# Performance work log

Measured on AMD Instinct MI355X. Metric: run time of the kernel, lower is better.

The kernel has to match this reference:

```python
import jax, jax.numpy as jnp
import numpy as np

B, T, D, H, K = 64, 2000, 512, 256, 5


def setup_inputs() -> dict:
    key = jax.random.key(0)
    ks = jax.random.split(key, 4)
    state = jax.random.normal(ks[0], (B, 1, D), dtype=jnp.float32)
    enc_z = jax.random.normal(ks[1], (B, T, D), dtype=jnp.float32)
    # small init scale keeps exp(param_net(state)) numerically tame
    W1 = jax.random.normal(ks[2], (D, H), dtype=jnp.float32) * 0.05
    b1 = jnp.zeros((H,), dtype=jnp.float32)
    W2 = jax.random.normal(ks[3], (H, 3 * K), dtype=jnp.float32) * 0.05
    b2 = jnp.zeros((3 * K,), dtype=jnp.float32)
    return {"state": state, "enc_z": enc_z, "W1": W1, "b1": b1, "W2": W2, "b2": b2}


def reference(state, enc_z, W1, b1, W2, b2):
    # param_net: Linear -> Tanh -> Linear, then exp (all params positive)
    h = jnp.tanh(state @ W1 + b1)                 # [B,1,H]
    params = jnp.exp(h @ W2 + b2)                 # [B,1,3K]
    means = params[..., 0::3]                     # [B,1,K]  (gather of indices 3i)
    scales = params[..., 1::3]                    # [B,1,K]  (indices 3i+1)
    w = params[..., 2::3]                         # [B,1,K]  (indices 3i+2)
    # NOTE: original applies softmax over dim=1 (the singleton dim) -> all ones.
    weights = jax.nn.softmax(w, axis=1)           # [B,1,K] == ones (faithful)
    t = enc_z.shape[1]
    j = jnp.arange(t, dtype=enc_z.dtype)[None, :, None]  # [1,T,1]
    cdf = lambda x: jax.nn.sigmoid((x - means) / scales)  # broadcasts -> [B,T,K]
    probs = weights * (cdf(j + 0.5) - cdf(j - 0.5))        # [B,T,K]
    align = jnp.sum(probs, axis=2)                          # [B,T]
    context = jnp.einsum('bt,btd->bd', align, enc_z)[:, None, :]  # [B,1,D]
    return context
```

## Files before the change

### kernel.cpp

```cpp
#include <hip/hip_runtime.h>
#include <math.h>

#define BB 64
#define TT 2000
#define DD 512
#define HH 256
#define KK 5
#define PP (3*KK)
#define D4 (DD/4)


__global__ __launch_bounds__(1024) void mlp_params_kernel(
    const float* __restrict__ state,
    const float* __restrict__ W1,
    const float* __restrict__ b1,
    const float* __restrict__ W2,
    const float* __restrict__ b2,
    float* __restrict__ ws_params)
{
    const int b     = blockIdx.x;
    const int tid   = threadIdx.x;
    const int q     = tid & 63;
    const int slice = tid >> 6;

    __shared__ float s_state[DD];
    __shared__ float s_part[16][HH];
    __shared__ float hs[HH];
    __shared__ float s_red[16][17];
    __shared__ float pr[PP];

    if (tid < DD) s_state[tid] = state[(size_t)b * DD + tid];
    __syncthreads();

    {
        const float4* w1v = (const float4*)W1;
        const int d0 = slice * 32;
        float4 acc = make_float4(0.f, 0.f, 0.f, 0.f);
        #pragma unroll 16
        for (int dd = 0; dd < 32; ++dd) {
            const int d    = d0 + dd;
            const float s  = s_state[d];
            const float4 w = w1v[(size_t)d * 64 + q];
            acc.x += s * w.x; acc.y += s * w.y;
            acc.z += s * w.z; acc.w += s * w.w;
        }
        s_part[slice][4*q+0] = acc.x;
        s_part[slice][4*q+1] = acc.y;
        s_part[slice][4*q+2] = acc.z;
        s_part[slice][4*q+3] = acc.w;
    }
    __syncthreads();

    if (tid < HH) {
        float a = b1[tid];
        #pragma unroll
        for (int s = 0; s < 16; ++s) a += s_part[s][tid];
        hs[tid] = tanhf(a);
    }
    __syncthreads();

    if (tid < 256) {
        const int p = tid >> 4;
        const int g = tid & 15;
        float a = 0.f;
        if (p < PP) {
            #pragma unroll
            for (int i = 0; i < 16; ++i)
                a += hs[g + 16*i] * W2[(size_t)(g + 16*i) * PP + p];
        }
        s_red[p][g] = a;
    }
    __syncthreads();
    if (tid < PP) {
        float a = b2[tid];
        #pragma unroll
        for (int g = 0; g < 16; ++g) a += s_red[tid][g];
        pr[tid] = expf(a);
    }
    __syncthreads();

    if (tid == 0) {
        float tc = 1.0f;
        #pragma unroll
        for (int k = 0; k < KK; ++k)
            tc = fmaxf(tc, pr[3*k] + 36.0f * pr[3*k+1] + 1.0f);
        ws_params[(size_t)b * 16 + 15] = tc;
    }
    if (tid < KK) {
        ws_params[(size_t)b * 16 + tid]     = pr[3*tid];
        ws_params[(size_t)b * 16 + 8 + tid] = 1.0f / pr[3*tid + 1];
    }
}

__global__ __launch_bounds__(512) void context_kernel(
    const float* __restrict__ enc_z,
    const float* __restrict__ ws_params,
    float* __restrict__ out)
{
    const int b   = blockIdx.x;
    const int tid = threadIdx.x;
    const int h   = tid >> 7;
    const int col = tid & 127;

    __shared__ float pr[16];
    __shared__ float al[TT];
    __shared__ float s_acc[4][DD];

    if (tid < 16) pr[tid] = ws_params[(size_t)b * 16 + tid];
    __syncthreads();

    const int Tact = min(TT, (int)ceilf(pr[15]));

    for (int t = tid; t < Tact; t += 512) {
        const float tf = (float)t;
        float a = 0.0f;
        #pragma unroll
        for (int k = 0; k < KK; ++k) {
            const float m  = pr[k];
            const float is = pr[8 + k];
            const float hi = (tf + 0.5f - m) * is;
            const float lo = (tf - 0.5f - m) * is;
            a += 1.0f / (1.0f + expf(-hi)) - 1.0f / (1.0f + expf(-lo));
        }
        al[t] = a;
    }
    __syncthreads();

    const float4* e4 = (const float4*)enc_z + (size_t)b * TT * D4 + col;
    float ax = 0.f, ay = 0.f, az = 0.f, aw = 0.f;
    #pragma unroll 4
    for (int t = h; t < Tact; t += 4) {
        const float a  = al[t];
        const float4 v = e4[(size_t)t * D4];
        ax += a * v.x; ay += a * v.y; az += a * v.z; aw += a * v.w;
    }
    s_acc[h][4*col+0] = ax;
    s_acc[h][4*col+1] = ay;
    s_acc[h][4*col+2] = az;
    s_acc[h][4*col+3] = aw;
    __syncthreads();

    if (tid < 128) {
        float4 r;
        r.x = s_acc[0][4*tid+0] + s_acc[1][4*tid+0] + s_acc[2][4*tid+0] + s_acc[3][4*tid+0];
        r.y = s_acc[0][4*tid+1] + s_acc[1][4*tid+1] + s_acc[2][4*tid+1] + s_acc[3][4*tid+1];
        r.z = s_acc[0][4*tid+2] + s_acc[1][4*tid+2] + s_acc[2][4*tid+2] + s_acc[3][4*tid+2];
        r.w = s_acc[0][4*tid+3] + s_acc[1][4*tid+3] + s_acc[2][4*tid+3] + s_acc[3][4*tid+3];
        ((float4*)out)[(size_t)b * D4 + tid] = r;
    }
}

extern "C" void kernel_launch(void* const* d_in, const int* in_sizes, int n_in,
                              void* d_out, int out_size, void* d_ws, size_t ws_size,
                              hipStream_t stream) {
    const float* state = (const float*)d_in[0];
    const float* enc_z = (const float*)d_in[1];
    const float* W1    = (const float*)d_in[2];
    const float* b1    = (const float*)d_in[3];
    const float* W2    = (const float*)d_in[4];
    const float* b2    = (const float*)d_in[5];
    float* out = (float*)d_out;

    float* ws_params = (float*)d_ws;

    mlp_params_kernel<<<BB, 1024, 0, stream>>>(state, W1, b1, W2, b2, ws_params);
    context_kernel<<<BB, 512, 0, stream>>>(enc_z, ws_params, out);
}
```

Baseline: 16.31 us.

## Split first MLP layer across blocks and fuse second layer into context kernel

The first linear layer now runs in a separate kernel launched with four blocks per batch row. Each block reduces one 128-wide slice of the input dimension and writes partial hidden sums to workspace. The tanh, the second layer, exp and the parameter extraction move into the start of the context kernel, so parameters no longer make a round trip through global memory. This spreads the W1 reads over more compute units and shortens the serial chain in the first kernel. In exchange, the context kernel repeats a small amount of MLP work per block.

Result: faster. 15.53 us (-4.8%).

```diff
diff --git a/kernel.cpp b/kernel.cpp
--- a/kernel.cpp
+++ b/kernel.cpp
@@ -8,54 +8,72 @@
 #define KK 5
 #define PP (3*KK)
 #define D4 (DD/4)
+#define NSL 4
 
 
-__global__ __launch_bounds__(1024) void mlp_params_kernel(
+__global__ __launch_bounds__(256) void h_partial_kernel(
     const float* __restrict__ state,
     const float* __restrict__ W1,
+    float* __restrict__ hpart)
+{
+    const int blk = blockIdx.x;
+    const int b   = blk >> 2;
+    const int s   = blk & 3;
+    const int tid = threadIdx.x;
+    const int q   = tid & 63;
+    const int r   = tid >> 6;
+
+    __shared__ float sst[128];
+    __shared__ float s_part[4][HH];
+
+    if (tid < 128) sst[tid] = state[(size_t)b * DD + s * 128 + tid];
+    __syncthreads();
+
+    const float4* w1v = (const float4*)W1;
+    float4 acc = make_float4(0.f, 0.f, 0.f, 0.f);
+    #pragma unroll 8
+    for (int it = 0; it < 32; ++it) {
+        const int dl = it * 4 + r;
+        const int d  = s * 128 + dl;
+        const float sv  = sst[dl];
+        const float4 w  = w1v[(size_t)d * 64 + q];
+        acc.x += sv * w.x; acc.y += sv * w.y;
+        acc.z += sv * w.z; acc.w += sv * w.w;
+    }
+    s_part[r][4*q+0] = acc.x;
+    s_part[r][4*q+1] = acc.y;
+    s_part[r][4*q+2] = acc.z;
+    s_part[r][4*q+3] = acc.w;
+    __syncthreads();
+
+    if (tid < HH)
+        hpart[((size_t)b * NSL + s) * HH + tid] =
+            s_part[0][tid] + s_part[1][tid] + s_part[2][tid] + s_part[3][tid];
+}
+
+__global__ __launch_bounds__(512) void context_kernel(
+    const float* __restrict__ enc_z,
+    const float* __restrict__ hpart,
     const float* __restrict__ b1,
     const float* __restrict__ W2,
     const float* __restrict__ b2,
-    float* __restrict__ ws_params)
+    float* __restrict__ out)
 {
-    const int b     = blockIdx.x;
-    const int tid   = threadIdx.x;
-    const int q     = tid & 63;
-    const int slice = tid >> 6;
+    const int b   = blockIdx.x;
+    const int tid = threadIdx.x;
+    const int h   = tid >> 7;
+    const int col = tid & 127;
 
-    __shared__ float s_state[DD];
-    __shared__ float s_part[16][HH];
     __shared__ float hs[HH];
     __shared__ float s_red[16][17];
     __shared__ float pr[PP];
-
-    if (tid < DD) s_state[tid] = state[(size_t)b * DD + tid];
-    __syncthreads();
-
-    {
-        const float4* w1v = (const float4*)W1;
-        const int d0 = slice * 32;
-        float4 acc = make_float4(0.f, 0.f, 0.f, 0.f);
-        #pragma unroll 16
-        for (int dd = 0; dd < 32; ++dd) {
-            const int d    = d0 + dd;
-            const float s  = s_state[d];
-            const float4 w = w1v[(size_t)d * 64 + q];
-            acc.x += s * w.x; acc.y += s * w.y;
-            acc.z += s * w.z; acc.w += s * w.w;
-        }
-        s_part[slice][4*q+0] = acc.x;
-        s_part[slice][4*q+1] = acc.y;
-        s_part[slice][4*q+2] = acc.z;
-        s_part[slice][4*q+3] = acc.w;
-    }
-    __syncthreads();
+    __shared__ float prm[16];
+    __shared__ float al[TT];
+    __shared__ float s_acc[4][DD];
 
     if (tid < HH) {
-        float a = b1[tid];
-        #pragma unroll
-        for (int s = 0; s < 16; ++s) a += s_part[s][tid];
-        hs[tid] = tanhf(a);
+        const float* hp = hpart + (size_t)b * NSL * HH + tid;
+        hs[tid] = tanhf(b1[tid] + hp[0] + hp[HH] + hp[2*HH] + hp[3*HH]);
     }
     __syncthreads();
 
@@ -78,46 +96,27 @@
         pr[tid] = expf(a);
     }
     __syncthreads();
-
     if (tid == 0) {
         float tc = 1.0f;
         #pragma unroll
         for (int k = 0; k < KK; ++k)
             tc = fmaxf(tc, pr[3*k] + 36.0f * pr[3*k+1] + 1.0f);
-        ws_params[(size_t)b * 16 + 15] = tc;
+        prm[15] = tc;
     }
     if (tid < KK) {
-        ws_params[(size_t)b * 16 + tid]     = pr[3*tid];
-        ws_params[(size_t)b * 16 + 8 + tid] = 1.0f / pr[3*tid + 1];
+        prm[tid]     = pr[3*tid];
+        prm[8 + tid] = 1.0f / pr[3*tid + 1];
     }
-}
-
-__global__ __launch_bounds__(512) void context_kernel(
-    const float* __restrict__ enc_z,
-    const float* __restrict__ ws_params,
-    float* __restrict__ out)
-{
-    const int b   = blockIdx.x;
-    const int tid = threadIdx.x;
-    const int h   = tid >> 7;
-    const int col = tid & 127;
-
-    __shared__ float pr[16];
-    __shared__ float al[TT];
-    __shared__ float s_acc[4][DD];
-
-    if (tid < 16) pr[tid] = ws_params[(size_t)b * 16 + tid];
     __syncthreads();
 
-    const int Tact = min(TT, (int)ceilf(pr[15]));
-
+    const int Tact = min(TT, (int)ceilf(prm[15]));
     for (int t = tid; t < Tact; t += 512) {
         const float tf = (float)t;
         float a = 0.0f;
         #pragma unroll
         for (int k = 0; k < KK; ++k) {
-            const float m  = pr[k];
-            const float is = pr[8 + k];
+            const float m  = prm[k];
+            const float is = prm[8 + k];
             const float hi = (tf + 0.5f - m) * is;
             const float lo = (tf - 0.5f - m) * is;
             a += 1.0f / (1.0f + expf(-hi)) - 1.0f / (1.0f + expf(-lo));
@@ -161,8 +160,8 @@
     const float* b2    = (const float*)d_in[5];
     float* out = (float*)d_out;
 
-    float* ws_params = (float*)d_ws;
+    float* ws_hpart = (float*)d_ws;
 
-    mlp_params_kernel<<<BB, 1024, 0, stream>>>(state, W1, b1, W2, b2, ws_params);
-    context_kernel<<<BB, 512, 0, stream>>>(enc_z, ws_params, out);
+    h_partial_kernel<<<BB * NSL, 256, 0, stream>>>(state, W1, ws_hpart);
+    context_kernel<<<BB, 512, 0, stream>>>(enc_z, ws_hpart, b1, W2, b2, out);
 }
```
